# Performance work log

Hardware: AMD Instinct MI355X
Metric: run time of the kernel (lower is better)

## Reference

```python
import jax, jax.numpy as jnp
import numpy as np
import math

B, NX, NY = 8, 1024, 1024
DIM_X = DIM_Y = DIM = 1024
H = 8


def layer_norm(x, g, b, eps=1e-5):
    mu = jnp.mean(x, axis=-1, keepdims=True)
    var = jnp.mean(jnp.square(x - mu), axis=-1, keepdims=True)
    return (x - mu) * jax.lax.rsqrt(var + eps) * g + b


def setup_inputs() -> dict:
    key = jax.random.key(0)
    ks = jax.random.split(key, 12)
    s = 1.0 / math.sqrt(DIM)
    return {
        "X": jax.random.normal(ks[0], (B, NX, DIM_X), jnp.float32),
        "Y": jax.random.normal(ks[1], (B, NY, DIM_Y), jnp.float32),
        "mask": jax.random.bernoulli(ks[2], 0.1, (B, NY)),  # True = masked out
        "Wq": jax.random.normal(ks[3], (DIM_X, DIM), jnp.float32) * s,
        "bq": jnp.zeros((DIM,), jnp.float32),
        "Wk": jax.random.normal(ks[4], (DIM_Y, DIM), jnp.float32) * s,
        "bk": jnp.zeros((DIM,), jnp.float32),
        "Wv": jax.random.normal(ks[5], (DIM_Y, DIM), jnp.float32) * s,
        "bv": jnp.zeros((DIM,), jnp.float32),
        "Wo": jax.random.normal(ks[6], (DIM, DIM), jnp.float32) * s,
        "bo": jnp.zeros((DIM,), jnp.float32),
        "g1": jnp.ones((DIM,), jnp.float32),
        "b1": jnp.zeros((DIM,), jnp.float32),
        "g2": jnp.ones((DIM,), jnp.float32),
        "b2": jnp.zeros((DIM,), jnp.float32),
    }


def reference(X, Y, mask, Wq, bq, Wk, bk, Wv, bv, Wo, bo, g1, b1, g2, b2):
    Q = X @ Wq + bq            # [B, NX, DIM]
    K = Y @ Wk + bk            # [B, NY, DIM]
    V = Y @ Wv + bv            # [B, NY, DIM]
    Dh = DIM // H
    Qh = Q.reshape(B, NX, H, Dh)
    Kh = K.reshape(B, NY, H, Dh)
    Vh = V.reshape(B, NY, H, Dh)
    # NOTE: original scales by sqrt(dim) (full model dim), not sqrt(head_dim)
    logits = jnp.einsum("bqhd,bkhd->bhqk", Qh, Kh) / math.sqrt(DIM)
    logits = jnp.where(mask[:, None, None, :], -jnp.inf, logits)
    A = jax.nn.softmax(logits, axis=-1)
    A = jnp.where(jnp.isnan(A), 0.0, A)  # fully-masked rows -> 0
    attn = jnp.einsum("bhqk,bkhd->bqhd", A, Vh).reshape(B, NX, DIM)
    O = layer_norm(Q + attn, g1, b1)
    O = layer_norm(O + jax.nn.relu(O @ Wo + bo), g2, b2)
    return O
```

## Files before the change

kernel.cpp:

```cpp
#include <hip/hip_runtime.h>
#include <stdint.h>


typedef unsigned short u16;
typedef unsigned int u32;
typedef __attribute__((ext_vector_type(8))) short s16x8;
typedef __attribute__((ext_vector_type(4))) float f32x4;
typedef __attribute__((ext_vector_type(16))) float f32x16;
typedef __attribute__((ext_vector_type(4))) u16 u16x4;

typedef __attribute__((address_space(1))) const void* as1cv;
typedef __attribute__((address_space(3))) void* as3v;

#define DEVINL __device__ __forceinline__

DEVINL u16 f2bf(float f) {
  union { float f; u32 u; } v; v.f = f;
  return (u16)((v.u + 0x7FFFu + ((v.u >> 16) & 1u)) >> 16);
}
DEVINL float bf2f(u16 x) {
  union { u32 u; float f; } v; v.u = ((u32)x) << 16;
  return v.f;
}
DEVINL u32 cvtpk_bf16(float lo, float hi) {
  u32 r;
  asm("v_cvt_pk_bf16_f32 %0, %1, %2" : "=v"(r) : "v"(lo), "v"(hi));
  return r;
}
DEVINL float fexp2(float x) {
  float r;
  asm("v_exp_f32 %0, %1" : "=v"(r) : "v"(x));
  return r;
}
DEVINL void gload_lds16(const void* g, void* l) {
  __builtin_amdgcn_global_load_lds((as1cv)g, (as3v)l, 16, 0, 0);
}
DEVINL f32x4 mfma16(s16x8 a, s16x8 b, f32x4 c) {
  return __builtin_amdgcn_mfma_f32_16x16x32_bf16(a, b, c, 0, 0, 0);
}
DEVINL f32x16 mfma32(s16x8 a, s16x8 b, f32x16 c) {
  return __builtin_amdgcn_mfma_f32_32x32x16_bf16(a, b, c, 0, 0, 0);
}

__global__ void prep_mask(const u32* __restrict__ mraw, float* __restrict__ maskb) {
  __shared__ int mode;
  int t = threadIdx.x;
  int fB = 0, fF = 0;
  for (int i = t; i < 2048; i += 256) {
    u32 v = mraw[i];
    if (v == 0x3F800000u) fF = 1;
    else if (v > 1u) fB = 1;
  }
  if (t == 0) mode = 0;
  __syncthreads();
  if (fB) atomicOr(&mode, 1);
  if (fF) atomicOr(&mode, 2);
  __syncthreads();
  int md = mode;
  int idx = blockIdx.x * 256 + t;
  int v;
  if (md & 1)       v = ((const unsigned char*)mraw)[idx] != 0;
  else if (md & 2)  v = ((const float*)mraw)[idx] != 0.0f;
  else              v = ((const int*)mraw)[idx] != 0;
  maskb[idx] = v ? -3e30f : -11.54156032f;
}

__global__ void cvt_f2bf2(const float* __restrict__ in0, u16* __restrict__ out0,
                          const float* __restrict__ in1, u16* __restrict__ out1,
                          int n4) {
  int i = blockIdx.x * blockDim.x + threadIdx.x;
  const float* in = in0;
  u16* out = out0;
  if (i >= n4) { i -= n4; in = in1; out = out1; }
  float4 v = *(const float4*)(in + (size_t)i * 4);
  u16x4 o; o[0] = f2bf(v.x); o[1] = f2bf(v.y); o[2] = f2bf(v.z); o[3] = f2bf(v.w);
  *(u16x4*)(out + (size_t)i * 4) = o;
}

__global__ void transpose_cvt(const float* __restrict__ W0, const float* __restrict__ W1,
                              const float* __restrict__ W2, const float* __restrict__ W3,
                              u16* __restrict__ T0, u16* __restrict__ T1,
                              u16* __restrict__ T2, u16* __restrict__ T3) {
  const float* W = (blockIdx.z == 0) ? W0 : (blockIdx.z == 1) ? W1 : (blockIdx.z == 2) ? W2 : W3;
  u16* T = (blockIdx.z == 0) ? T0 : (blockIdx.z == 1) ? T1 : (blockIdx.z == 2) ? T2 : T3;
  __shared__ float tile[32][33];
  int tx = threadIdx.x, ty = threadIdx.y;
  int N0 = blockIdx.x << 5, K0 = blockIdx.y << 5;
#pragma unroll
  for (int i = 0; i < 4; ++i)
    tile[ty + i * 8][tx] = W[(size_t)(K0 + ty + i * 8) * 1024 + N0 + tx];
  __syncthreads();
#pragma unroll
  for (int i = 0; i < 4; ++i)
    T[(size_t)(N0 + ty + i * 8) * 1024 + K0 + tx] = f2bf(tile[tx][ty + i * 8]);
}

template <int MODE>
__global__ __launch_bounds__(256, 2) void gemm_nt(
    const u16* __restrict__ A, const u16* __restrict__ Bt,
    const float* __restrict__ bias, float* __restrict__ outF,
    u16* __restrict__ outBF, const u16* __restrict__ residBF) {
  __shared__ u16 lA[128 * 64];
  __shared__ u16 lB[128 * 64];

  const int id = blockIdx.x;
  const int cpx = gridDim.x >> 3;
  const int swz = (id & 7) * cpx + (id >> 3);
  const int mb = swz >> 3;
  const int nb = swz & 7;

  const int tid = threadIdx.x;
  const int w = tid >> 6, l = tid & 63;
  const int wm = w >> 1, wn = w & 1;
  const int lrow = l & 15, lk = l >> 4;

  const int sr = l >> 3;
  const int scol = ((l & 7) << 4) ^ (sr << 4);
  const char* gA = (const char*)A + (size_t)(mb * 128) * 2048;
  const char* gB = (const char*)Bt + (size_t)(nb * 128) * 2048;

  f32x4 acc[4][4];
#pragma unroll
  for (int i = 0; i < 4; ++i)
#pragma unroll
    for (int j = 0; j < 4; ++j) acc[i][j] = f32x4{0.f, 0.f, 0.f, 0.f};

  for (int kt = 0; kt < 16; ++kt) {
    const int kb = kt * 128;
#pragma unroll
    for (int c = 0; c < 4; ++c) {
      int row = (w * 4 + c) * 8 + sr;
      gload_lds16(gA + (size_t)row * 2048 + kb + scol, (char*)lA + (w * 4 + c) * 1024);
      gload_lds16(gB + (size_t)row * 2048 + kb + scol, (char*)lB + (w * 4 + c) * 1024);
    }
    __syncthreads();
#pragma unroll
    for (int kc = 0; kc < 2; ++kc) {
      s16x8 af[4], bfr[4];
#pragma unroll
      for (int mi = 0; mi < 4; ++mi) {
        int row = wm * 64 + mi * 16 + lrow;
        int off = row * 128 + ((lk * 16 + kc * 64) ^ ((row & 7) << 4));
        af[mi] = *(const s16x8*)((const char*)lA + off);
      }
#pragma unroll
      for (int ni = 0; ni < 4; ++ni) {
        int row = wn * 64 + ni * 16 + lrow;
        int off = row * 128 + ((lk * 16 + kc * 64) ^ ((row & 7) << 4));
        bfr[ni] = *(const s16x8*)((const char*)lB + off);
      }
      __builtin_amdgcn_s_setprio(1);
#pragma unroll
      for (int mi = 0; mi < 4; ++mi)
#pragma unroll
        for (int ni = 0; ni < 4; ++ni)
          acc[mi][ni] = mfma16(af[mi], bfr[ni], acc[mi][ni]);
      __builtin_amdgcn_s_setprio(0);
    }
    __syncthreads();
  }

  const int growb = mb * 128 + wm * 64;
  const int gcolb = nb * 128 + wn * 64;
  float bs[4];
#pragma unroll
  for (int ni = 0; ni < 4; ++ni) bs[ni] = bias[gcolb + ni * 16 + lrow];

#pragma unroll
  for (int mi = 0; mi < 4; ++mi) {
    const int grow0 = growb + mi * 16 + lk * 4;
#pragma unroll
    for (int ni = 0; ni < 4; ++ni) {
      const int gcol = gcolb + ni * 16 + lrow;
      if (MODE == 2) {
        u16x4 pk;
#pragma unroll
        for (int r = 0; r < 4; ++r) pk[r] = f2bf(acc[mi][ni][r] + bs[ni]);
        size_t flat = ((size_t)((grow0 >> 10) << 10) + gcol) * 1024 + (grow0 & 1023);
        *(u16x4*)(outBF + flat) = pk;
      } else {
#pragma unroll
        for (int r = 0; r < 4; ++r) {
          float v = acc[mi][ni][r] + bs[ni];
          size_t idx = (size_t)(grow0 + r) * 1024 + gcol;
          if (MODE == 1) { outBF[idx] = f2bf(v); }
          if (MODE == 3) { outBF[idx] = f2bf(bf2f(residBF[idx]) + fmaxf(v, 0.f)); }
        }
      }
    }
  }
}

__global__ __launch_bounds__(256, 2) void attn_fwd(
    const u16* __restrict__ Qbf, const u16* __restrict__ Kbf,
    const u16* __restrict__ Vt, const float* __restrict__ maskb,
    u16* __restrict__ attnO) {
  __shared__ u16 lK[2][64 * 128];
  __shared__ u16 lV[2][128 * 64];
  __shared__ float lM[1024];

  const int id = blockIdx.x;
  const int xcd = id & 7, seq = id >> 3;
  const int bh = xcd * 8 + (seq >> 3);
  const int qb = seq & 7;
  const int b = bh >> 3, h = bh & 7;
  const int tid = threadIdx.x;
  const int w = tid >> 6, l = tid & 63;
  const int q32 = l & 31, hi = l >> 5;

  const u16* Qrow = Qbf + ((size_t)(b * 1024 + qb * 128 + w * 32 + q32)) * 1024 + h * 128;
  s16x8 qf[8];
#pragma unroll
  for (int dc = 0; dc < 8; ++dc) qf[dc] = *(const s16x8*)(Qrow + dc * 16 + hi * 8);

  const int srK = l >> 4, slK = l & 15;
  const int srV = l >> 3, slV = l & 7;
  int soK[4], soV[4];
#pragma unroll
  for (int c = 0; c < 4; ++c) {
    int rowK = (w * 4 + c) * 4 + srK;
    soK[c] = rowK * 2048 + ((slK << 4) ^ ((rowK & 15) << 4));
    int dV = (w * 4 + c) * 8 + srV;
    soV[c] = dV * 2048 + ((slV << 4) ^ ((dV & 7) << 4));
  }
  const char* pgK = (const char*)(Kbf + ((size_t)(b * 1024)) * 1024 + h * 128);
  const char* pgV = (const char*)(Vt + ((size_t)(b * 1024 + h * 128)) * 1024);

  int loK[8], loV[4];
#pragma unroll
  for (int c = 0; c < 8; ++c)
    loK[c] = q32 * 256 + ((c * 32 + hi * 16) ^ ((q32 & 15) << 4));
#pragma unroll
  for (int c = 0; c < 4; ++c)
    loV[c] = q32 * 128 + ((c * 32 + hi * 16) ^ ((q32 & 7) << 4));

  if (w == 0) {
#pragma unroll
    for (int c = 0; c < 4; ++c)
      gload_lds16(maskb + b * 1024 + c * 256 + l * 4, (char*)lM + c * 1024);
  }

  float l_ = 0.f;
  f32x16 oacc[4];
#pragma unroll
  for (int i = 0; i < 4; ++i)
#pragma unroll
    for (int r = 0; r < 16; ++r) oacc[i][r] = 0.f;

  const float SCL = 0.04508422f;

#define ATT_STAGE(NXT, TN)                                                    \
  {                                                                           \
    const char* pk_ = pgK + (size_t)(TN)*131072;                              \
    const char* pv_ = pgV + (size_t)(TN)*128;                                 \
    _Pragma("unroll")                                                         \
    for (int c = 0; c < 4; ++c) {                                             \
      gload_lds16(pk_ + soK[c], (char*)lK[NXT] + w * 4096 + c * 1024);        \
      gload_lds16(pv_ + soV[c], (char*)lV[NXT] + w * 4096 + c * 1024);        \
    }                                                                         \
  }

#define ATT_COMPUTE(CUR, PMT)                                                 \
  {                                                                           \
    f32x16 sc[2];                                                             \
    _Pragma("unroll")                                                         \
    for (int kb = 0; kb < 2; ++kb)                                            \
      _Pragma("unroll")                                                       \
      for (int r = 0; r < 16; ++r) sc[kb][r] = 0.f;                           \
    __builtin_amdgcn_s_setprio(1);                                            \
    _Pragma("unroll")                                                         \
    for (int dc = 0; dc < 8; ++dc) {                                          \
      _Pragma("unroll")                                                       \
      for (int kb = 0; kb < 2; ++kb) {                                        \
        s16x8 kf = *(const s16x8*)((const char*)lK[CUR] + loK[dc] + kb * 8192); \
        sc[kb] = mfma32(kf, qf[dc], sc[kb]);                                  \
      }                                                                       \
    }                                                                         \
    __builtin_amdgcn_s_setprio(0);                                            \
    float rs = 0.f;                                                           \
    _Pragma("unroll")                                                         \
    for (int kb = 0; kb < 2; ++kb) {                                          \
      f32x4 mv[4];                                                            \
      _Pragma("unroll")                                                       \
      for (int g = 0; g < 4; ++g)                                             \
        mv[g] = *(const f32x4*)((PMT) + kb * 128 + g * 32);                   \
      _Pragma("unroll")                                                       \
      for (int r = 0; r < 16; ++r) {                                          \
        float pe = fexp2(fmaf(sc[kb][r], SCL, mv[r >> 2][r & 3]));            \
        sc[kb][r] = pe;                                                       \
        rs += pe;                                                             \
      }                                                                       \
    }                                                                         \
    rs += __shfl_xor(rs, 32);                                                 \
    l_ += rs;                                                                 \
    u32 pk[2][8];                                                             \
    _Pragma("unroll")                                                         \
    for (int kb = 0; kb < 2; ++kb)                                            \
      _Pragma("unroll")                                                       \
      for (int r2 = 0; r2 < 8; ++r2)                                          \
        pk[kb][r2] = cvtpk_bf16(sc[kb][2 * r2], sc[kb][2 * r2 + 1]);          \
    _Pragma("unroll")                                                         \
    for (int kc = 0; kc < 4; ++kc) {                                          \
      const int kb = kc >> 1;                                                 \
      const int ra = (kc & 1) * 4;                                            \
      u32 x0 = pk[kb][ra + 0], y0 = pk[kb][ra + 2];                           \
      u32 x1 = pk[kb][ra + 1], y1 = pk[kb][ra + 3];                           \
      asm("v_permlane32_swap_b32 %0, %1" : "+v"(x0), "+v"(y0));               \
      asm("v_permlane32_swap_b32 %0, %1" : "+v"(x1), "+v"(y1));               \
      union { u32 u[4]; s16x8 v; } pa;                                        \
      pa.u[0] = x0; pa.u[1] = x1; pa.u[2] = y0; pa.u[3] = y1;                 \
      __builtin_amdgcn_s_setprio(1);                                          \
      _Pragma("unroll")                                                       \
      for (int nb = 0; nb < 4; ++nb) {                                        \
        s16x8 vb = *(const s16x8*)((const char*)lV[CUR] + loV[kc] + nb * 4096); \
        oacc[nb] = mfma32(pa.v, vb, oacc[nb]);                                \
      }                                                                       \
      __builtin_amdgcn_s_setprio(0);                                          \
    }                                                                         \
  }

  const char* pM0 = (const char*)lM + hi * 16;

  ATT_STAGE(0, 0);
  __syncthreads();
  for (int it = 0; it < 7; ++it) {
    const char* pMa = pM0 + it * 512;
    ATT_STAGE(1, 2 * it + 1);
    ATT_COMPUTE(0, pMa);
    __syncthreads();
    ATT_STAGE(0, 2 * it + 2);
    ATT_COMPUTE(1, pMa + 256);
    __syncthreads();
  }
  {
    const char* pMa = pM0 + 7 * 512;
    ATT_STAGE(1, 15);
    ATT_COMPUTE(0, pMa);
    __syncthreads();
    ATT_COMPUTE(1, pMa + 256);
  }
#undef ATT_STAGE
#undef ATT_COMPUTE

  float inv = (l_ > 1e-20f) ? (1.0f / l_) : 0.f;
  u16* obase = attnO + ((size_t)(b * 1024 + qb * 128 + w * 32)) * 1024 + h * 128;
#pragma unroll
  for (int r = 0; r < 16; ++r) {
    int qr = (r & 3) + 8 * (r >> 2) + 4 * hi;
    float iv = __shfl(inv, qr);
#pragma unroll
    for (int nb = 0; nb < 4; ++nb)
      obase[(size_t)qr * 1024 + nb * 32 + q32] = f2bf(oacc[nb][r] * iv);
  }
}

__global__ __launch_bounds__(256) void ln_fused(
    const float* __restrict__ aF, const u16* __restrict__ aBF,
    const u16* __restrict__ baddBF, const float* __restrict__ g,
    const float* __restrict__ bt, float* __restrict__ outF,
    u16* __restrict__ outBF) {
  const int row = blockIdx.x;
  const int c = threadIdx.x << 2;
  const size_t base = (size_t)row * 1024 + c;
  float4 h;
  if (aF) {
    h = *(const float4*)(aF + base);
  } else {
    u16x4 u = *(const u16x4*)(aBF + base);
    h.x = bf2f(u[0]); h.y = bf2f(u[1]); h.z = bf2f(u[2]); h.w = bf2f(u[3]);
  }
  if (baddBF) {
    u16x4 u = *(const u16x4*)(baddBF + base);
    h.x += bf2f(u[0]); h.y += bf2f(u[1]); h.z += bf2f(u[2]); h.w += bf2f(u[3]);
  }
  float s = (h.x + h.y) + (h.z + h.w);
  float q = (h.x * h.x + h.y * h.y) + (h.z * h.z + h.w * h.w);
#pragma unroll
  for (int msk = 1; msk < 64; msk <<= 1) {
    s += __shfl_xor(s, msk);
    q += __shfl_xor(q, msk);
  }
  __shared__ float sh[8];
  const int w = threadIdx.x >> 6;
  if ((threadIdx.x & 63) == 0) { sh[w] = s; sh[4 + w] = q; }
  __syncthreads();
  s = (sh[0] + sh[1]) + (sh[2] + sh[3]);
  q = (sh[4] + sh[5]) + (sh[6] + sh[7]);
  const float mu = s * (1.f / 1024.f);
  const float var = q * (1.f / 1024.f) - mu * mu;
  const float rstd = rsqrtf(var + 1e-5f);
  const float4 gv = *(const float4*)(g + c);
  const float4 bv = *(const float4*)(bt + c);
  float4 o;
  o.x = (h.x - mu) * rstd * gv.x + bv.x;
  o.y = (h.y - mu) * rstd * gv.y + bv.y;
  o.z = (h.z - mu) * rstd * gv.z + bv.z;
  o.w = (h.w - mu) * rstd * gv.w + bv.w;
  if (outF) *(float4*)(outF + base) = o;
  if (outBF) {
    u16x4 ub; ub[0] = f2bf(o.x); ub[1] = f2bf(o.y); ub[2] = f2bf(o.z); ub[3] = f2bf(o.w);
    *(u16x4*)(outBF + base) = ub;
  }
}

extern "C" void kernel_launch(void* const* d_in, const int* in_sizes, int n_in,
                              void* d_out, int out_size, void* d_ws, size_t ws_size,
                              hipStream_t stream) {
  const float* X  = (const float*)d_in[0];
  const float* Y  = (const float*)d_in[1];
  const void*  mask = d_in[2];
  const float* Wq = (const float*)d_in[3];
  const float* bq = (const float*)d_in[4];
  const float* Wk = (const float*)d_in[5];
  const float* bk = (const float*)d_in[6];
  const float* Wv = (const float*)d_in[7];
  const float* bv = (const float*)d_in[8];
  const float* Wo = (const float*)d_in[9];
  const float* bo = (const float*)d_in[10];
  const float* g1 = (const float*)d_in[11];
  const float* b1 = (const float*)d_in[12];
  const float* g2 = (const float*)d_in[13];
  const float* b2 = (const float*)d_in[14];
  float* out = (float*)d_out;

  char* ws = (char*)d_ws;
  const size_t MB = 1024ull * 1024ull;
  u16* Xbf    = (u16*)(ws + 0);
  u16* Ybf    = (u16*)(ws + 16 * MB);
  u16* Qbf    = (u16*)(ws + 32 * MB);
  u16* Kbf    = (u16*)(ws + 48 * MB);
  u16* Vt     = (u16*)(ws + 64 * MB);
  u16* attnbf = (u16*)(ws + 80 * MB);
  u16* Wqt = (u16*)(ws + 112 * MB);
  u16* Wkt = (u16*)(ws + 114 * MB);
  u16* Wvt = (u16*)(ws + 116 * MB);
  u16* Wot = (u16*)(ws + 118 * MB);
  float* maskb = (float*)(ws + 120 * MB);
  u16* Rbf = Kbf;
  u16* O1bf = Xbf;

  prep_mask<<<dim3(32), dim3(256), 0, stream>>>((const u32*)mask, maskb);
  cvt_f2bf2<<<dim3(16384), dim3(256), 0, stream>>>(X, Xbf, Y, Ybf, 2097152);
  transpose_cvt<<<dim3(32, 32, 4), dim3(32, 8), 0, stream>>>(Wq, Wk, Wv, Wo, Wqt, Wkt, Wvt, Wot);

  gemm_nt<1><<<dim3(512), dim3(256), 0, stream>>>(Xbf, Wqt, bq, nullptr, Qbf, nullptr);
  gemm_nt<1><<<dim3(512), dim3(256), 0, stream>>>(Ybf, Wkt, bk, nullptr, Kbf, nullptr);
  gemm_nt<2><<<dim3(512), dim3(256), 0, stream>>>(Ybf, Wvt, bv, nullptr, Vt, nullptr);

  attn_fwd<<<dim3(512), dim3(256), 0, stream>>>(Qbf, Kbf, Vt, maskb, attnbf);

  ln_fused<<<dim3(8192), dim3(256), 0, stream>>>(nullptr, Qbf, attnbf, g1, b1, nullptr, O1bf);
  gemm_nt<3><<<dim3(512), dim3(256), 0, stream>>>(O1bf, Wot, bo, nullptr, Rbf, O1bf);
  ln_fused<<<dim3(8192), dim3(256), 0, stream>>>(nullptr, Rbf, nullptr, g2, b2, out, nullptr);
}
```

Baseline: 182.9 us.

## Single-buffer V tile with split K/V staging to fit three blocks per CU

The attention kernel drops the V double buffer and stages K and V separately. Each tile issues its V load before the QK^T stage, prefetches the next K during softmax, and waits with explicit vmcnt counts and raw barriers instead of __syncthreads. It also changes the V LDS swizzle layout and raises the launch bound to 3 blocks per CU so the smaller LDS footprint can give more occupancy. In exchange, the V load latency is exposed inside each tile, there are more barriers per tile, and the register budget is tighter.

New measurement: 277.1 us. +51.5%, slower.

```diff
diff --git a/kernel.cpp b/kernel.cpp
--- a/kernel.cpp
+++ b/kernel.cpp
@@ -40,6 +40,15 @@
 }
 DEVINL f32x16 mfma32(s16x8 a, s16x8 b, f32x16 c) {
   return __builtin_amdgcn_mfma_f32_32x32x16_bf16(a, b, c, 0, 0, 0);
+}
+template <int N> DEVINL void wait_vm() {
+  asm volatile("s_waitcnt vmcnt(%0)" :: "i"(N) : "memory");
+  __builtin_amdgcn_sched_barrier(0);
+}
+DEVINL void barrier_raw() {
+  __builtin_amdgcn_sched_barrier(0);
+  __builtin_amdgcn_s_barrier();
+  __builtin_amdgcn_sched_barrier(0);
 }
 
 __global__ void prep_mask(const u32* __restrict__ mraw, float* __restrict__ maskb) {
@@ -191,12 +200,12 @@
   }
 }
 
-__global__ __launch_bounds__(256, 2) void attn_fwd(
+__global__ __launch_bounds__(256, 3) void attn_fwd(
     const u16* __restrict__ Qbf, const u16* __restrict__ Kbf,
     const u16* __restrict__ Vt, const float* __restrict__ maskb,
     u16* __restrict__ attnO) {
   __shared__ u16 lK[2][64 * 128];
-  __shared__ u16 lV[2][128 * 64];
+  __shared__ u16 lV[128 * 64];
   __shared__ float lM[1024];
 
   const int id = blockIdx.x;
@@ -214,14 +223,15 @@
   for (int dc = 0; dc < 8; ++dc) qf[dc] = *(const s16x8*)(Qrow + dc * 16 + hi * 8);
 
   const int srK = l >> 4, slK = l & 15;
-  const int srV = l >> 3, slV = l & 7;
   int soK[4], soV[4];
 #pragma unroll
   for (int c = 0; c < 4; ++c) {
     int rowK = (w * 4 + c) * 4 + srK;
     soK[c] = rowK * 2048 + ((slK << 4) ^ ((rowK & 15) << 4));
-    int dV = (w * 4 + c) * 8 + srV;
-    soV[c] = dV * 2048 + ((slV << 4) ^ ((dV & 7) << 4));
+    int pairid = (w * 4 + c) * 4 + (l >> 4);
+    int u = (l & 15) ^ (pairid & 15);
+    int d = pairid * 2 + (u >> 3);
+    soV[c] = d * 2048 + (u & 7) * 16;
   }
   const char* pgK = (const char*)(Kbf + ((size_t)(b * 1024)) * 1024 + h * 128);
   const char* pgV = (const char*)(Vt + ((size_t)(b * 1024 + h * 128)) * 1024);
@@ -232,13 +242,17 @@
     loK[c] = q32 * 256 + ((c * 32 + hi * 16) ^ ((q32 & 15) << 4));
 #pragma unroll
   for (int c = 0; c < 4; ++c)
-    loV[c] = q32 * 128 + ((c * 32 + hi * 16) ^ ((q32 & 7) << 4));
+    loV[c] = (q32 >> 1) * 256 +
+             (((((q32 & 1) << 3) | (c * 2 + hi)) ^ ((q32 >> 1) & 15)) << 4);
 
   if (w == 0) {
 #pragma unroll
     for (int c = 0; c < 4; ++c)
       gload_lds16(maskb + b * 1024 + c * 256 + l * 4, (char*)lM + c * 1024);
   }
+#pragma unroll
+  for (int c = 0; c < 4; ++c)
+    gload_lds16(pgK + soK[c], (char*)lK[0] + w * 4096 + c * 1024);
 
   float l_ = 0.f;
   f32x16 oacc[4];
@@ -248,20 +262,27 @@
     for (int r = 0; r < 16; ++r) oacc[i][r] = 0.f;
 
   const float SCL = 0.04508422f;
-
-#define ATT_STAGE(NXT, TN)                                                    \
+  const char* pM0 = (const char*)lM + hi * 16;
+
+#define STAGE_K(TN, BUF)                                                      \
   {                                                                           \
     const char* pk_ = pgK + (size_t)(TN)*131072;                              \
+    _Pragma("unroll")                                                         \
+    for (int c = 0; c < 4; ++c)                                               \
+      gload_lds16(pk_ + soK[c], (char*)lK[BUF] + w * 4096 + c * 1024);        \
+  }
+#define STAGE_V(TN)                                                           \
+  {                                                                           \
     const char* pv_ = pgV + (size_t)(TN)*128;                                 \
     _Pragma("unroll")                                                         \
-    for (int c = 0; c < 4; ++c) {                                             \
-      gload_lds16(pk_ + soK[c], (char*)lK[NXT] + w * 4096 + c * 1024);        \
-      gload_lds16(pv_ + soV[c], (char*)lV[NXT] + w * 4096 + c * 1024);        \
-    }                                                                         \
-  }
-
-#define ATT_COMPUTE(CUR, PMT)                                                 \
+    for (int c = 0; c < 4; ++c)                                               \
+      gload_lds16(pv_ + soV[c], (char*)lV + w * 4096 + c * 1024);             \
+  }
+
+#define ATT_TILE(T, CUR, FIRST, LAST)                                         \
   {                                                                           \
+    STAGE_V(T);                                                               \
+    if (FIRST) { wait_vm<4>(); barrier_raw(); }                               \
     f32x16 sc[2];                                                             \
     _Pragma("unroll")                                                         \
     for (int kb = 0; kb < 2; ++kb)                                            \
@@ -277,13 +298,14 @@
       }                                                                       \
     }                                                                         \
     __builtin_amdgcn_s_setprio(0);                                            \
+    const char* pMa = pM0 + (T)*256;                                          \
     float rs = 0.f;                                                           \
     _Pragma("unroll")                                                         \
     for (int kb = 0; kb < 2; ++kb) {                                          \
       f32x4 mv[4];                                                            \
       _Pragma("unroll")                                                       \
       for (int g = 0; g < 4; ++g)                                             \
-        mv[g] = *(const f32x4*)((PMT) + kb * 128 + g * 32);                   \
+        mv[g] = *(const f32x4*)(pMa + kb * 128 + g * 32);                     \
       _Pragma("unroll")                                                       \
       for (int r = 0; r < 16; ++r) {                                          \
         float pe = fexp2(fmaf(sc[kb][r], SCL, mv[r >> 2][r & 3]));            \
@@ -299,6 +321,9 @@
       _Pragma("unroll")                                                       \
       for (int r2 = 0; r2 < 8; ++r2)                                          \
         pk[kb][r2] = cvtpk_bf16(sc[kb][2 * r2], sc[kb][2 * r2 + 1]);          \
+    if (!(LAST)) STAGE_K((T) + 1, (CUR) ^ 1);                                 \
+    if (LAST) wait_vm<0>(); else wait_vm<4>();                                \
+    barrier_raw();                                                            \
     _Pragma("unroll")                                                         \
     for (int kc = 0; kc < 4; ++kc) {                                          \
       const int kb = kc >> 1;                                                 \
@@ -312,35 +337,33 @@
       __builtin_amdgcn_s_setprio(1);                                          \
       _Pragma("unroll")                                                       \
       for (int nb = 0; nb < 4; ++nb) {                                        \
-        s16x8 vb = *(const s16x8*)((const char*)lV[CUR] + loV[kc] + nb * 4096); \
+        s16x8 vb = *(const s16x8*)((const char*)lV + loV[kc] + nb * 4096);    \
         oacc[nb] = mfma32(pa.v, vb, oacc[nb]);                                \
       }                                                                       \
       __builtin_amdgcn_s_setprio(0);                                          \
     }                                                                         \
-  }
-
-  const char* pM0 = (const char*)lM + hi * 16;
-
-  ATT_STAGE(0, 0);
-  __syncthreads();
-  for (int it = 0; it < 7; ++it) {
-    const char* pMa = pM0 + it * 512;
-    ATT_STAGE(1, 2 * it + 1);
-    ATT_COMPUTE(0, pMa);
-    __syncthreads();
-    ATT_STAGE(0, 2 * it + 2);
-    ATT_COMPUTE(1, pMa + 256);
-    __syncthreads();
-  }
-  {
-    const char* pMa = pM0 + 7 * 512;
-    ATT_STAGE(1, 15);
-    ATT_COMPUTE(0, pMa);
-    __syncthreads();
-    ATT_COMPUTE(1, pMa + 256);
-  }
-#undef ATT_STAGE
-#undef ATT_COMPUTE
+    if (!(LAST)) { wait_vm<0>(); barrier_raw(); }                             \
+  }
+
+  ATT_TILE(0, 0, true, false);
+  ATT_TILE(1, 1, false, false);
+  ATT_TILE(2, 0, false, false);
+  ATT_TILE(3, 1, false, false);
+  ATT_TILE(4, 0, false, false);
+  ATT_TILE(5, 1, false, false);
+  ATT_TILE(6, 0, false, false);
+  ATT_TILE(7, 1, false, false);
+  ATT_TILE(8, 0, false, false);
+  ATT_TILE(9, 1, false, false);
+  ATT_TILE(10, 0, false, false);
+  ATT_TILE(11, 1, false, false);
+  ATT_TILE(12, 0, false, false);
+  ATT_TILE(13, 1, false, false);
+  ATT_TILE(14, 0, false, false);
+  ATT_TILE(15, 1, false, true);
+#undef ATT_TILE
+#undef STAGE_K
+#undef STAGE_V
 
   float inv = (l_ > 1e-20f) ? (1.0f / l_) : 0.f;
   u16* obase = attnO + ((size_t)(b * 1024 + qb * 128 + w * 32)) * 1024 + h * 128;
```

## Merge prep kernels into one launch and re-swizzle V LDS layout

Applied to the files above, without the earlier changes.

Folds the three preprocessing kernels (mask prep, X/Y bf16 conversion, weight transpose) into a single kernel that dispatches on block index, cutting two launches and the gaps between them. Separately changes the LDS swizzle for V tiles in attention so that pairs of rows share a 256-byte line with a 16-way XOR pattern, aimed at reducing bank conflicts on V reads. The V layout change has to stay consistent between the global-to-LDS writes and the fragment reads, and a mistake there would silently corrupt results.

Measured after the change: 178.5 us. 2.4% less time.

```diff
diff --git a/kernel.cpp b/kernel.cpp
--- a/kernel.cpp
+++ b/kernel.cpp
@@ -42,9 +42,45 @@
   return __builtin_amdgcn_mfma_f32_32x32x16_bf16(a, b, c, 0, 0, 0);
 }
 
-__global__ void prep_mask(const u32* __restrict__ mraw, float* __restrict__ maskb) {
+__global__ __launch_bounds__(256) void prep_all(
+    const float* __restrict__ X, u16* __restrict__ Xbf,
+    const float* __restrict__ Y, u16* __restrict__ Ybf,
+    const float* __restrict__ W0, const float* __restrict__ W1,
+    const float* __restrict__ W2, const float* __restrict__ W3,
+    u16* __restrict__ T0, u16* __restrict__ T1,
+    u16* __restrict__ T2, u16* __restrict__ T3,
+    const u32* __restrict__ mraw, float* __restrict__ maskb) {
+  const int bid = blockIdx.x;
+  const int t = threadIdx.x;
+  if (bid < 16384) {
+    int i = bid * 256 + t;
+    const float* in = X;
+    u16* out = Xbf;
+    if (i >= 2097152) { i -= 2097152; in = Y; out = Ybf; }
+    float4 v = *(const float4*)(in + (size_t)i * 4);
+    u16x4 o; o[0] = f2bf(v.x); o[1] = f2bf(v.y); o[2] = f2bf(v.z); o[3] = f2bf(v.w);
+    *(u16x4*)(out + (size_t)i * 4) = o;
+    return;
+  }
+  if (bid < 20480) {
+    const int r = bid - 16384;
+    const int z = r >> 10, tile = r & 1023;
+    const int bx = tile & 31, by = tile >> 5;
+    const float* W = (z == 0) ? W0 : (z == 1) ? W1 : (z == 2) ? W2 : W3;
+    u16* T = (z == 0) ? T0 : (z == 1) ? T1 : (z == 2) ? T2 : T3;
+    __shared__ float tl[32][33];
+    const int tx = t & 31, ty = t >> 5;
+    const int N0 = bx << 5, K0 = by << 5;
+#pragma unroll
+    for (int i = 0; i < 4; ++i)
+      tl[ty + i * 8][tx] = W[(size_t)(K0 + ty + i * 8) * 1024 + N0 + tx];
+    __syncthreads();
+#pragma unroll
+    for (int i = 0; i < 4; ++i)
+      T[(size_t)(N0 + ty + i * 8) * 1024 + K0 + tx] = f2bf(tl[tx][ty + i * 8]);
+    return;
+  }
   __shared__ int mode;
-  int t = threadIdx.x;
   int fB = 0, fF = 0;
   for (int i = t; i < 2048; i += 256) {
     u32 v = mraw[i];
@@ -56,43 +92,13 @@
   if (fB) atomicOr(&mode, 1);
   if (fF) atomicOr(&mode, 2);
   __syncthreads();
-  int md = mode;
-  int idx = blockIdx.x * 256 + t;
+  const int md = mode;
+  const int idx = (bid - 20480) * 256 + t;
   int v;
   if (md & 1)       v = ((const unsigned char*)mraw)[idx] != 0;
   else if (md & 2)  v = ((const float*)mraw)[idx] != 0.0f;
   else              v = ((const int*)mraw)[idx] != 0;
   maskb[idx] = v ? -3e30f : -11.54156032f;
-}
-
-__global__ void cvt_f2bf2(const float* __restrict__ in0, u16* __restrict__ out0,
-                          const float* __restrict__ in1, u16* __restrict__ out1,
-                          int n4) {
-  int i = blockIdx.x * blockDim.x + threadIdx.x;
-  const float* in = in0;
-  u16* out = out0;
-  if (i >= n4) { i -= n4; in = in1; out = out1; }
-  float4 v = *(const float4*)(in + (size_t)i * 4);
-  u16x4 o; o[0] = f2bf(v.x); o[1] = f2bf(v.y); o[2] = f2bf(v.z); o[3] = f2bf(v.w);
-  *(u16x4*)(out + (size_t)i * 4) = o;
-}
-
-__global__ void transpose_cvt(const float* __restrict__ W0, const float* __restrict__ W1,
-                              const float* __restrict__ W2, const float* __restrict__ W3,
-                              u16* __restrict__ T0, u16* __restrict__ T1,
-                              u16* __restrict__ T2, u16* __restrict__ T3) {
-  const float* W = (blockIdx.z == 0) ? W0 : (blockIdx.z == 1) ? W1 : (blockIdx.z == 2) ? W2 : W3;
-  u16* T = (blockIdx.z == 0) ? T0 : (blockIdx.z == 1) ? T1 : (blockIdx.z == 2) ? T2 : T3;
-  __shared__ float tile[32][33];
-  int tx = threadIdx.x, ty = threadIdx.y;
-  int N0 = blockIdx.x << 5, K0 = blockIdx.y << 5;
-#pragma unroll
-  for (int i = 0; i < 4; ++i)
-    tile[ty + i * 8][tx] = W[(size_t)(K0 + ty + i * 8) * 1024 + N0 + tx];
-  __syncthreads();
-#pragma unroll
-  for (int i = 0; i < 4; ++i)
-    T[(size_t)(N0 + ty + i * 8) * 1024 + K0 + tx] = f2bf(tile[tx][ty + i * 8]);
 }
 
 template <int MODE>
@@ -214,14 +220,15 @@
   for (int dc = 0; dc < 8; ++dc) qf[dc] = *(const s16x8*)(Qrow + dc * 16 + hi * 8);
 
   const int srK = l >> 4, slK = l & 15;
-  const int srV = l >> 3, slV = l & 7;
   int soK[4], soV[4];
 #pragma unroll
   for (int c = 0; c < 4; ++c) {
     int rowK = (w * 4 + c) * 4 + srK;
     soK[c] = rowK * 2048 + ((slK << 4) ^ ((rowK & 15) << 4));
-    int dV = (w * 4 + c) * 8 + srV;
-    soV[c] = dV * 2048 + ((slV << 4) ^ ((dV & 7) << 4));
+    int pairid = (w * 4 + c) * 4 + (l >> 4);
+    int u = (l & 15) ^ (pairid & 15);
+    int d = pairid * 2 + (u >> 3);
+    soV[c] = d * 2048 + (u & 7) * 16;
   }
   const char* pgK = (const char*)(Kbf + ((size_t)(b * 1024)) * 1024 + h * 128);
   const char* pgV = (const char*)(Vt + ((size_t)(b * 1024 + h * 128)) * 1024);
@@ -232,7 +239,8 @@
     loK[c] = q32 * 256 + ((c * 32 + hi * 16) ^ ((q32 & 15) << 4));
 #pragma unroll
   for (int c = 0; c < 4; ++c)
-    loV[c] = q32 * 128 + ((c * 32 + hi * 16) ^ ((q32 & 7) << 4));
+    loV[c] = (q32 >> 1) * 256 +
+             (((((q32 & 1) << 3) | (c * 2 + hi)) ^ ((q32 >> 1) & 15)) << 4);
 
   if (w == 0) {
 #pragma unroll
@@ -439,9 +447,9 @@
   u16* Rbf = Kbf;
   u16* O1bf = Xbf;
 
-  prep_mask<<<dim3(32), dim3(256), 0, stream>>>((const u32*)mask, maskb);
-  cvt_f2bf2<<<dim3(16384), dim3(256), 0, stream>>>(X, Xbf, Y, Ybf, 2097152);
-  transpose_cvt<<<dim3(32, 32, 4), dim3(32, 8), 0, stream>>>(Wq, Wk, Wv, Wo, Wqt, Wkt, Wvt, Wot);
+  prep_all<<<dim3(20512), dim3(256), 0, stream>>>(
+      X, Xbf, Y, Ybf, Wq, Wk, Wv, Wo, Wqt, Wkt, Wvt, Wot,
+      (const u32*)mask, maskb);
 
   gemm_nt<1><<<dim3(512), dim3(256), 0, stream>>>(Xbf, Wqt, bq, nullptr, Qbf, nullptr);
   gemm_nt<1><<<dim3(512), dim3(256), 0, stream>>>(Ybf, Wkt, bk, nullptr, Kbf, nullptr);
```
